# Performance work log

Measured on AMD Instinct MI355X. Metric: run time of the kernel, lower is better.

The kernel has to match this reference:

```python
import jax, jax.numpy as jnp
import numpy as np

HID = 1024
NH = 16
HD = 64
INTER = 2816
EPS = 1e-5


def _rms_norm(x, eps=EPS):
    x32 = x.astype(jnp.float32)
    var = jnp.mean(x32 * x32, axis=-1, keepdims=True)
    return (x32 * jax.lax.rsqrt(var + eps)).astype(x.dtype)


def _rotate_half(x):
    x1, x2 = jnp.split(x, 2, axis=-1)
    return jnp.concatenate([-x2, x1], axis=-1)


def setup_inputs() -> dict:
    key = jax.random.key(0)
    ks = jax.random.split(key, 6)
    B, S = 1, 2048
    # real RoPE tables: [S, HD]
    inv_freq = 1.0 / (10000.0 ** (np.arange(0, HD, 2, dtype=np.float32) / HD))
    t = np.arange(S, dtype=np.float32)
    freqs = np.outer(t, inv_freq)  # [S, HD/2]
    emb = np.concatenate([freqs, freqs], axis=-1)  # [S, HD]
    cos = jnp.asarray(np.cos(emb))
    sin = jnp.asarray(np.sin(emb))
    sc = 0.02
    return {
        "cos": cos,
        "sin": sin,
        "hidden_states": jax.random.normal(ks[0], (B, S, HID), jnp.float32),
        "attn_bias": jax.random.normal(ks[1], (B, NH, S, S), jnp.float32) * 0.1,
        "w_qkv": jax.random.normal(ks[2], (HID, (NH + 2 * NH) * HD), jnp.float32) * sc,
        "w_o": jax.random.normal(ks[3], (NH * HD, HID), jnp.float32) * sc,
        "w_gate_up": jax.random.normal(ks[4], (HID, 2 * INTER), jnp.float32) * sc,
        "w_down": jax.random.normal(ks[5], (INTER, HID), jnp.float32) * sc,
    }


def _attention(cos, sin, x, attn_bias, w_qkv, w_o):
    B, S, _ = x.shape
    qkv = (x @ w_qkv).reshape(B, S, 3 * NH, HD)
    q = qkv[:, :, :NH]          # [B,S,H,D]
    k = qkv[:, :, NH:2 * NH]
    v = qkv[:, :, 2 * NH:]
    c = cos[None, :, None, :]
    s = sin[None, :, None, :]
    q = q * c + _rotate_half(q) * s
    k = k * c + _rotate_half(k) * s
    scale = HD ** -0.5
    scores = jnp.einsum('bqhd,bkhd->bhqk', q, k) * scale + attn_bias
    attn = jax.nn.softmax(scores.astype(jnp.float32), axis=-1).astype(q.dtype)
    out = jnp.einsum('bhqk,bkhd->bqhd', attn, v).reshape(B, S, NH * HD)
    return out @ w_o


def _swiglu(x, w_gate_up, w_down):
    gu = x @ w_gate_up
    gate, up = jnp.split(gu, 2, axis=-1)
    return (jax.nn.silu(gate) * up) @ w_down


def reference(cos, sin, hidden_states, attn_bias, w_qkv, w_o, w_gate_up, w_down):
    x = hidden_states
    x = _rms_norm(x + _attention(cos, sin, x, attn_bias, w_qkv, w_o))
    x = _rms_norm(x + _swiglu(x, w_gate_up, w_down))
    return x
```

## Files before the change

### kernel.cpp

```cpp
#include <hip/hip_runtime.h>
#include <stdint.h>

using u16 = unsigned short;
typedef __bf16 bf16x8 __attribute__((ext_vector_type(8)));
typedef float f32x4 __attribute__((ext_vector_type(4)));

__device__ __forceinline__ u16 f2bf(float f) {
  union { float f; uint32_t u; } v; v.f = f;
  uint32_t r = v.u + 0x7fffu + ((v.u >> 16) & 1u);
  return (u16)(r >> 16);
}
__device__ __forceinline__ float bf2f(u16 h) {
  union { uint32_t u; float f; } v; v.u = ((uint32_t)h) << 16;
  return v.f;
}
__device__ __forceinline__ bf16x8 ldb8(const u16* p) {
  return *reinterpret_cast<const bf16x8*>(p);
}
__device__ __forceinline__ void gload_lds16(const void* g, void* l) {
  __builtin_amdgcn_global_load_lds(
      (const __attribute__((address_space(1))) void*)g,
      (__attribute__((address_space(3))) void*)l, 16, 0, 0);
}

__global__ __launch_bounds__(256) void prep_kernel(
    const float* __restrict__ w_qkv, const float* __restrict__ w_o,
    const float* __restrict__ w_gu, const float* __restrict__ w_down,
    const float* __restrict__ hidden, u16* __restrict__ wqkv_t,
    u16* __restrict__ wo_t, u16* __restrict__ wgu_t, u16* __restrict__ wd_t,
    u16* __restrict__ xb) {
  const int b = blockIdx.x;
  const int t = threadIdx.x;

  if (b >= 12544) {
    int idx = (b - 12544) * 256 + t;
    float4 v = *(const float4*)(hidden + (size_t)idx * 4);
    ushort4 o;
    o.x = f2bf(v.x); o.y = f2bf(v.y); o.z = f2bf(v.z); o.w = f2bf(v.w);
    *(ushort4*)(xb + (size_t)idx * 4) = o;
    return;
  }

  const float* W;
  u16* Wt;
  int N, K, lb;
  bool perm = false;
  if (b < 3072)      { W = w_qkv; Wt = wqkv_t; N = 3072; K = 1024; lb = b; }
  else if (b < 4096) { W = w_o;   Wt = wo_t;   N = 1024; K = 1024; lb = b - 3072; }
  else if (b < 9728) { W = w_gu;  Wt = wgu_t;  N = 5632; K = 1024; lb = b - 4096; perm = true; }
  else               { W = w_down; Wt = wd_t;  N = 1024; K = 2816; lb = b - 9728; }

  const int nx = N >> 5;
  const int n0 = (lb % nx) * 32, k0 = (lb / nx) * 32;
  const int tx = t & 31, ty = t >> 5;

  __shared__ u16 tile[32][33];
  const int nc = n0 + tx;
  const int src_col = perm ? (((nc & 1) == 0) ? (nc >> 1) : 2816 + (nc >> 1))
                           : nc;
#pragma unroll
  for (int i = 0; i < 32; i += 8)
    tile[ty + i][tx] = f2bf(W[(size_t)(k0 + ty + i) * N + src_col]);
  __syncthreads();
#pragma unroll
  for (int i = 0; i < 32; i += 8)
    Wt[(size_t)(n0 + ty + i) * K + k0 + tx] = tile[tx][ty + i];
}

__global__ __launch_bounds__(256) void gemm_qkv_rope(
    const u16* __restrict__ A, const u16* __restrict__ Bt,
    const float* __restrict__ cosb, const float* __restrict__ sinb,
    u16* __restrict__ qb, u16* __restrict__ kb, u16* __restrict__ vt,
    int M, int N, int K) {
  __shared__ __align__(16) u16 As[128 * 32];
  __shared__ __align__(16) u16 Bs[128 * 32];
  __shared__ u16 vbuf[4][64][17];
  const int tid = threadIdx.x;
  const int w = tid >> 6, lane = tid & 63;
  const int wr = w >> 1, wc = w & 1;
  const int r16 = lane & 15, g = lane >> 4;
  const int nwg = gridDim.x * gridDim.y;
  const int idx = blockIdx.y * gridDim.x + blockIdx.x;
  const int swz = (idx & 7) * (nwg >> 3) + (idx >> 3);
  const int m0 = (swz / gridDim.x) * 128, n0 = (swz % gridDim.x) * 128;
  const int ldrow = lane >> 2;
  const int ldk = (lane & 3) * 8;

  f32x4 acc[4][4] = {};

  for (int kt = 0; kt < K; kt += 32) {
#pragma unroll
    for (int i = 0; i < 2; ++i) {
      int chunk = w * 2 + i;
      int row = chunk * 16 + ldrow;
      gload_lds16(A + (size_t)(m0 + row) * K + kt + ldk, &As[chunk * 512]);
      gload_lds16(Bt + (size_t)(n0 + row) * K + kt + ldk, &Bs[chunk * 512]);
    }
    __syncthreads();
    bf16x8 a[4], b[4];
#pragma unroll
    for (int mt = 0; mt < 4; ++mt)
      a[mt] = ldb8(&As[(wr * 64 + mt * 16 + r16) * 32 + g * 8]);
#pragma unroll
    for (int nt = 0; nt < 4; ++nt)
      b[nt] = ldb8(&Bs[(wc * 64 + nt * 16 + r16) * 32 + g * 8]);
#pragma unroll
    for (int mt = 0; mt < 4; ++mt)
#pragma unroll
      for (int nt = 0; nt < 4; ++nt)
        acc[mt][nt] = __builtin_amdgcn_mfma_f32_16x16x32_bf16(
            a[mt], b[nt], acc[mt][nt], 0, 0, 0);
    __syncthreads();
  }

  const int type = n0 >> 10;
  const int head = ((n0 & 1023) >> 6) + wc;
  if (type < 2) {
    u16* outp = type == 0 ? qb : kb;
    const float qs = type == 0 ? 0.125f : 1.0f;
#pragma unroll
    for (int mt = 0; mt < 4; ++mt)
#pragma unroll
      for (int r = 0; r < 4; ++r) {
        const int srow = m0 + wr * 64 + mt * 16 + g * 4 + r;
#pragma unroll
        for (int nt = 0; nt < 4; ++nt) {
          const int d = nt * 16 + r16;
          float cv = cosb[srow * 64 + d];
          float sv = sinb[srow * 64 + d];
          float sgn = nt < 2 ? -1.f : 1.f;
          float val = acc[mt][nt][r] * cv + sgn * acc[mt][nt ^ 2][r] * sv;
          outp[((size_t)head * 2048 + srow) * 64 + d] = f2bf(val * qs);
        }
      }
  } else {
    const int s_base = m0 + wr * 64;
    const int d_lo = lane >> 4;
    (void)d_lo;
    const int dl = lane >> 2;
    const int sblk = (lane & 3) * 16;
#pragma unroll
    for (int nt = 0; nt < 4; ++nt) {
#pragma unroll
      for (int mt = 0; mt < 4; ++mt)
#pragma unroll
        for (int r = 0; r < 4; ++r)
          vbuf[w][mt * 16 + g * 4 + r][r16] = f2bf(acc[mt][nt][r]);
      u16* dst =
          vt + ((size_t)(head * 64 + nt * 16 + dl)) * 2048 + s_base + sblk;
#pragma unroll
      for (int jj = 0; jj < 4; ++jj) {
        ushort4 ov;
        ov.x = vbuf[w][sblk + jj * 4 + 0][dl];
        ov.y = vbuf[w][sblk + jj * 4 + 1][dl];
        ov.z = vbuf[w][sblk + jj * 4 + 2][dl];
        ov.w = vbuf[w][sblk + jj * 4 + 3][dl];
        *(ushort4*)(dst + jj * 4) = ov;
      }
    }
  }
}

__global__ __launch_bounds__(256) void gemm_bt_swiglu(
    const u16* __restrict__ A, const u16* __restrict__ Bt,
    u16* __restrict__ Hb, int M, int N, int K) {
  __shared__ __align__(16) u16 As[128 * 32];
  __shared__ __align__(16) u16 Bs[128 * 32];
  const int tid = threadIdx.x;
  const int w = tid >> 6, lane = tid & 63;
  const int wr = w >> 1, wc = w & 1;
  const int r16 = lane & 15, g = lane >> 4;
  const int nwg = gridDim.x * gridDim.y;
  const int idx = blockIdx.y * gridDim.x + blockIdx.x;
  const int swz = (idx & 7) * (nwg >> 3) + (idx >> 3);
  const int m0 = (swz / gridDim.x) * 128, n0 = (swz % gridDim.x) * 128;
  const int ldrow = lane >> 2;
  const int ldk = (lane & 3) * 8;

  f32x4 acc[4][4] = {};

  for (int kt = 0; kt < K; kt += 32) {
#pragma unroll
    for (int i = 0; i < 2; ++i) {
      int chunk = w * 2 + i;
      int row = chunk * 16 + ldrow;
      gload_lds16(A + (size_t)(m0 + row) * K + kt + ldk, &As[chunk * 512]);
      gload_lds16(Bt + (size_t)(n0 + row) * K + kt + ldk, &Bs[chunk * 512]);
    }
    __syncthreads();
    bf16x8 a[4], b[4];
#pragma unroll
    for (int mt = 0; mt < 4; ++mt)
      a[mt] = ldb8(&As[(wr * 64 + mt * 16 + r16) * 32 + g * 8]);
#pragma unroll
    for (int nt = 0; nt < 4; ++nt)
      b[nt] = ldb8(&Bs[(wc * 64 + nt * 16 + r16) * 32 + g * 8]);
#pragma unroll
    for (int mt = 0; mt < 4; ++mt)
#pragma unroll
      for (int nt = 0; nt < 4; ++nt)
        acc[mt][nt] = __builtin_amdgcn_mfma_f32_16x16x32_bf16(
            a[mt], b[nt], acc[mt][nt], 0, 0, 0);
    __syncthreads();
  }
#pragma unroll
  for (int mt = 0; mt < 4; ++mt)
#pragma unroll
    for (int nt = 0; nt < 4; ++nt)
#pragma unroll
      for (int r = 0; r < 4; ++r) {
        float val = acc[mt][nt][r];
        float other = __shfl_xor(val, 1);
        if ((r16 & 1) == 0) {
          float o = val / (1.f + __expf(-val)) * other;
          int row = m0 + wr * 64 + mt * 16 + g * 4 + r;
          int col = n0 + wc * 64 + nt * 16 + r16;
          Hb[(size_t)row * 2816 + (col >> 1)] = f2bf(o);
        }
      }
}

__global__ __launch_bounds__(256) void gemm_bt64(
    const u16* __restrict__ A, const u16* __restrict__ Bt,
    u16* __restrict__ C, int M, int N, int K) {
  __shared__ __align__(16) u16 As[64 * 32];
  __shared__ __align__(16) u16 Bs[128 * 32];
  const int tid = threadIdx.x;
  const int w = tid >> 6, lane = tid & 63;
  const int wr = w >> 1, wc = w & 1;
  const int r16 = lane & 15, g = lane >> 4;
  const int nwg = gridDim.x * gridDim.y;
  const int idx = blockIdx.y * gridDim.x + blockIdx.x;
  const int swz = (idx & 7) * (nwg >> 3) + (idx >> 3);
  const int m0 = (swz / gridDim.x) * 64, n0 = (swz % gridDim.x) * 128;
  const int ldrow = lane >> 2;
  const int ldk = (lane & 3) * 8;

  f32x4 acc[2][4] = {};

  for (int kt = 0; kt < K; kt += 32) {
#pragma unroll
    for (int i = 0; i < 3; ++i) {
      int chunk = w * 3 + i;
      if (chunk < 4) {
        int row = chunk * 16 + ldrow;
        gload_lds16(A + (size_t)(m0 + row) * K + kt + ldk, &As[chunk * 512]);
      } else {
        int cb = chunk - 4;
        int row = cb * 16 + ldrow;
        gload_lds16(Bt + (size_t)(n0 + row) * K + kt + ldk, &Bs[cb * 512]);
      }
    }
    __syncthreads();
    bf16x8 a[2], b[4];
#pragma unroll
    for (int mt = 0; mt < 2; ++mt)
      a[mt] = ldb8(&As[(wr * 32 + mt * 16 + r16) * 32 + g * 8]);
#pragma unroll
    for (int nt = 0; nt < 4; ++nt)
      b[nt] = ldb8(&Bs[(wc * 64 + nt * 16 + r16) * 32 + g * 8]);
#pragma unroll
    for (int mt = 0; mt < 2; ++mt)
#pragma unroll
      for (int nt = 0; nt < 4; ++nt)
        acc[mt][nt] = __builtin_amdgcn_mfma_f32_16x16x32_bf16(
            a[mt], b[nt], acc[mt][nt], 0, 0, 0);
    __syncthreads();
  }
#pragma unroll
  for (int mt = 0; mt < 2; ++mt)
#pragma unroll
    for (int nt = 0; nt < 4; ++nt)
#pragma unroll
      for (int r = 0; r < 4; ++r) {
        int row = m0 + wr * 32 + mt * 16 + g * 4 + r;
        int col = n0 + wc * 64 + nt * 16 + r16;
        C[(size_t)row * N + col] = f2bf(acc[mt][nt][r]);
      }
}

__global__ __launch_bounds__(256, 2) void attn_kernel(
    const u16* __restrict__ qb, const u16* __restrict__ kb,
    const u16* __restrict__ vt, const float* __restrict__ bias,
    u16* __restrict__ attnb) {
  const int bid = blockIdx.x;
  const int swz = (bid & 7) * 64 + (bid >> 3);
  const int h = swz >> 5;
  const int qt = swz & 31;
  const int tid = threadIdx.x;
  const int w = tid >> 6;
  const int lane = tid & 63;
  const int r16 = lane & 15, g = lane >> 4;

  __shared__ __align__(16) u16 P_lds[4][16 * 32];
  __shared__ float acc_s[4][16][64];
  __shared__ float m_s[4][16], l_s[4][16];

  bf16x8 qf0[4], qf1[4];
#pragma unroll
  for (int st = 0; st < 4; ++st) {
    const u16* qrow =
        qb + ((size_t)h * 2048 + qt * 64 + st * 16 + r16) * 64;
    qf0[st] = ldb8(qrow + g * 8);
    qf1[st] = ldb8(qrow + 32 + g * 8);
  }

  f32x4 acc[4][4] = {};
  float m[4][4], lsum[4][4];
#pragma unroll
  for (int st = 0; st < 4; ++st)
#pragma unroll
    for (int r = 0; r < 4; ++r) { m[st][r] = -1e30f; lsum[st][r] = 0.f; }

  const float* bbase = bias + ((size_t)h * 2048 + qt * 64) * 2048;

  const int kv0 = w * 512, kv1 = kv0 + 512;
  for (int kt = kv0; kt < kv1; kt += 32) {
    bf16x8 ka[2], kc[2];
#pragma unroll
    for (int c = 0; c < 2; ++c) {
      const u16* krow = kb + ((size_t)h * 2048 + kt + c * 16 + r16) * 64;
      ka[c] = ldb8(krow + g * 8);
      kc[c] = ldb8(krow + 32 + g * 8);
    }
    bf16x8 vf[4];
#pragma unroll
    for (int nt = 0; nt < 4; ++nt)
      vf[nt] =
          ldb8(vt + ((size_t)h * 64 + nt * 16 + r16) * 2048 + kt + g * 8);

#pragma unroll
    for (int st = 0; st < 4; ++st) {
      float bv[2][4];
#pragma unroll
      for (int c = 0; c < 2; ++c)
#pragma unroll
        for (int r = 0; r < 4; ++r)
          bv[c][r] = bbase[(size_t)(st * 16 + g * 4 + r) * 2048 + kt +
                           c * 16 + r16];

      f32x4 sc[2];
#pragma unroll
      for (int c = 0; c < 2; ++c) {
        f32x4 z = {0.f, 0.f, 0.f, 0.f};
        f32x4 t =
            __builtin_amdgcn_mfma_f32_16x16x32_bf16(qf0[st], ka[c], z, 0, 0, 0);
        sc[c] =
            __builtin_amdgcn_mfma_f32_16x16x32_bf16(qf1[st], kc[c], t, 0, 0, 0);
      }
#pragma unroll
      for (int c = 0; c < 2; ++c)
#pragma unroll
        for (int r = 0; r < 4; ++r)
          sc[c][r] += bv[c][r];

      float mnew[4];
#pragma unroll
      for (int r = 0; r < 4; ++r) {
        float t = fmaxf(sc[0][r], sc[1][r]);
        t = fmaxf(t, __shfl_xor(t, 1));
        t = fmaxf(t, __shfl_xor(t, 2));
        t = fmaxf(t, __shfl_xor(t, 4));
        t = fmaxf(t, __shfl_xor(t, 8));
        mnew[r] = fmaxf(m[st][r], t);
      }
#pragma unroll
      for (int r = 0; r < 4; ++r) {
        float p0 = __expf(sc[0][r] - mnew[r]);
        float p1 = __expf(sc[1][r] - mnew[r]);
        sc[0][r] = p0; sc[1][r] = p1;
        float alpha = __expf(m[st][r] - mnew[r]);
        lsum[st][r] = lsum[st][r] * alpha + (p0 + p1);
        m[st][r] = mnew[r];
#pragma unroll
        for (int nt = 0; nt < 4; ++nt) acc[st][nt][r] *= alpha;
      }
#pragma unroll
      for (int c = 0; c < 2; ++c)
#pragma unroll
        for (int r = 0; r < 4; ++r)
          P_lds[w][(g * 4 + r) * 32 + c * 16 + r16] = f2bf(sc[c][r]);
      bf16x8 pf = ldb8(&P_lds[w][r16 * 32 + g * 8]);
#pragma unroll
      for (int nt = 0; nt < 4; ++nt)
        acc[st][nt] = __builtin_amdgcn_mfma_f32_16x16x32_bf16(
            pf, vf[nt], acc[st][nt], 0, 0, 0);
    }
  }

#pragma unroll
  for (int st = 0; st < 4; ++st) {
    __syncthreads();
#pragma unroll
    for (int nt = 0; nt < 4; ++nt)
#pragma unroll
      for (int r = 0; r < 4; ++r)
        acc_s[w][g * 4 + r][nt * 16 + r16] = acc[st][nt][r];
    if (r16 == 0) {
#pragma unroll
      for (int r = 0; r < 4; ++r) m_s[w][g * 4 + r] = m[st][r];
    }
#pragma unroll
    for (int r = 0; r < 4; ++r) {
      float t = lsum[st][r];
      t += __shfl_xor(t, 1);
      t += __shfl_xor(t, 2);
      t += __shfl_xor(t, 4);
      t += __shfl_xor(t, 8);
      if (r16 == 0) l_s[w][g * 4 + r] = t;
    }
    __syncthreads();

    const int row = tid >> 4;
    const int col4 = (tid & 15) * 4;
    float m0v = m_s[0][row], m1v = m_s[1][row], m2v = m_s[2][row],
          m3v = m_s[3][row];
    float mm = fmaxf(fmaxf(m0v, m1v), fmaxf(m2v, m3v));
    float s0 = __expf(m0v - mm), s1 = __expf(m1v - mm);
    float s2 = __expf(m2v - mm), s3 = __expf(m3v - mm);
    float ltot = l_s[0][row] * s0 + l_s[1][row] * s1 + l_s[2][row] * s2 +
                 l_s[3][row] * s3;
    float inv = 1.f / ltot;
    ushort4 ov;
    u16* outp =
        attnb + (size_t)(qt * 64 + st * 16 + row) * 1024 + h * 64 + col4;
#pragma unroll
    for (int j = 0; j < 4; ++j) {
      float v = acc_s[0][row][col4 + j] * s0 + acc_s[1][row][col4 + j] * s1 +
                acc_s[2][row][col4 + j] * s2 + acc_s[3][row][col4 + j] * s3;
      ((u16*)&ov)[j] = f2bf(v * inv);
    }
    *(ushort4*)outp = ov;
  }
}

__global__ __launch_bounds__(256) void addnorm_kernel(
    const float* __restrict__ resid, const u16* __restrict__ delta,
    float* __restrict__ outf, u16* __restrict__ outb) {
  int row = blockIdx.x, tid = threadIdx.x;
  size_t base = (size_t)row * 1024 + tid * 4;
  float4 rv = *(const float4*)(resid + base);
  ushort4 dv = *(const ushort4*)(delta + base);
  float x0 = rv.x + bf2f(dv.x);
  float x1 = rv.y + bf2f(dv.y);
  float x2 = rv.z + bf2f(dv.z);
  float x3 = rv.w + bf2f(dv.w);
  float ss = x0 * x0 + x1 * x1 + x2 * x2 + x3 * x3;
#pragma unroll
  for (int sh = 32; sh >= 1; sh >>= 1) ss += __shfl_xor(ss, sh);
  __shared__ float red[4];
  if ((tid & 63) == 0) red[tid >> 6] = ss;
  __syncthreads();
  float tot = red[0] + red[1] + red[2] + red[3];
  float rstd = rsqrtf(tot * (1.0f / 1024.0f) + 1e-5f);
  float4 ov;
  ov.x = x0 * rstd; ov.y = x1 * rstd; ov.z = x2 * rstd; ov.w = x3 * rstd;
  *(float4*)(outf + base) = ov;
  if (outb) {
    ushort4 ob;
    ob.x = f2bf(ov.x); ob.y = f2bf(ov.y); ob.z = f2bf(ov.z); ob.w = f2bf(ov.w);
    *(ushort4*)(outb + base) = ob;
  }
}

extern "C" void kernel_launch(void* const* d_in, const int* in_sizes, int n_in,
                              void* d_out, int out_size, void* d_ws,
                              size_t ws_size, hipStream_t stream) {
  (void)in_sizes; (void)n_in; (void)out_size; (void)ws_size;
  const float* cosb  = (const float*)d_in[0];
  const float* sinb  = (const float*)d_in[1];
  const float* hidden = (const float*)d_in[2];
  const float* bias  = (const float*)d_in[3];
  const float* w_qkv = (const float*)d_in[4];
  const float* w_o   = (const float*)d_in[5];
  const float* w_gu  = (const float*)d_in[6];
  const float* w_down = (const float*)d_in[7];
  float* out = (float*)d_out;

  char* p = (char*)d_ws;
  auto alloc = [&](size_t bytes) {
    void* r = (void*)p;
    p += (bytes + 255) & ~(size_t)255;
    return r;
  };
  u16* wqkv_t = (u16*)alloc((size_t)3072 * 1024 * 2);
  u16* wo_t   = (u16*)alloc((size_t)1024 * 1024 * 2);
  u16* wgu_t  = (u16*)alloc((size_t)5632 * 1024 * 2);
  u16* wd_t   = (u16*)alloc((size_t)1024 * 2816 * 2);
  u16* xb     = (u16*)alloc((size_t)2048 * 1024 * 2);
  u16* qb     = (u16*)alloc((size_t)16 * 2048 * 64 * 2);
  u16* kb     = (u16*)alloc((size_t)16 * 2048 * 64 * 2);
  u16* vt     = (u16*)alloc((size_t)16 * 2048 * 64 * 2);
  u16* attnb  = (u16*)alloc((size_t)2048 * 1024 * 2);
  u16* ob     = (u16*)alloc((size_t)2048 * 1024 * 2);
  float* x1f  = (float*)alloc((size_t)2048 * 1024 * 4);
  u16* x1b    = (u16*)alloc((size_t)2048 * 1024 * 2);
  u16* hb     = (u16*)alloc((size_t)2048 * 2816 * 2);
  u16* mlpb   = (u16*)alloc((size_t)2048 * 1024 * 2);

  prep_kernel<<<14592, 256, 0, stream>>>(w_qkv, w_o, w_gu, w_down, hidden,
                                         wqkv_t, wo_t, wgu_t, wd_t, xb);

  gemm_qkv_rope<<<dim3(3072 / 128, 2048 / 128), 256, 0, stream>>>(
      xb, wqkv_t, cosb, sinb, qb, kb, vt, 2048, 3072, 1024);
  attn_kernel<<<512, 256, 0, stream>>>(qb, kb, vt, bias, attnb);
  gemm_bt64<<<dim3(1024 / 128, 2048 / 64), 256, 0, stream>>>(attnb, wo_t, ob, 2048, 1024, 1024);
  addnorm_kernel<<<2048, 256, 0, stream>>>(hidden, ob, x1f, x1b);
  gemm_bt_swiglu<<<dim3(5632 / 128, 2048 / 128), 256, 0, stream>>>(x1b, wgu_t, hb, 2048, 5632, 1024);
  gemm_bt64<<<dim3(1024 / 128, 2048 / 64), 256, 0, stream>>>(hb, wd_t, mlpb, 2048, 1024, 2816);
  addnorm_kernel<<<2048, 256, 0, stream>>>(x1f, mlpb, out, nullptr);
}
```

Measured before the change: 288.6 us.

## Shrink output GEMM tiles to 64x64 and widen attention KV step to 64

The o-proj and down-proj GEMMs move from 64x128 to 64x64 tiles, doubling the grid to 512 workgroups so more of the CUs are busy, at the cost of less operand reuse per tile. The attention inner loop now handles 64 keys per iteration instead of 32. K and V fragments are loaded inside the per-subtile loop, and the bias is read directly rather than prefetched, which halves the number of softmax max/rescale passes per key. This changes the register pressure and load scheduling in the attention kernel, and may add redundant K/V reloads across the four query subtiles.

Result: slower. 592.0 us (+105.1%).

```diff
diff --git a/kernel.cpp b/kernel.cpp
--- a/kernel.cpp
+++ b/kernel.cpp
@@ -135,8 +135,6 @@
       }
   } else {
     const int s_base = m0 + wr * 64;
-    const int d_lo = lane >> 4;
-    (void)d_lo;
     const int dl = lane >> 2;
     const int sblk = (lane & 3) * 16;
 #pragma unroll
@@ -220,11 +218,11 @@
       }
 }
 
-__global__ __launch_bounds__(256) void gemm_bt64(
+__global__ __launch_bounds__(256) void gemm_bt6464(
     const u16* __restrict__ A, const u16* __restrict__ Bt,
     u16* __restrict__ C, int M, int N, int K) {
   __shared__ __align__(16) u16 As[64 * 32];
-  __shared__ __align__(16) u16 Bs[128 * 32];
+  __shared__ __align__(16) u16 Bs[64 * 32];
   const int tid = threadIdx.x;
   const int w = tid >> 6, lane = tid & 63;
   const int wr = w >> 1, wc = w & 1;
@@ -232,16 +230,16 @@
   const int nwg = gridDim.x * gridDim.y;
   const int idx = blockIdx.y * gridDim.x + blockIdx.x;
   const int swz = (idx & 7) * (nwg >> 3) + (idx >> 3);
-  const int m0 = (swz / gridDim.x) * 64, n0 = (swz % gridDim.x) * 128;
+  const int m0 = (swz / gridDim.x) * 64, n0 = (swz % gridDim.x) * 64;
   const int ldrow = lane >> 2;
   const int ldk = (lane & 3) * 8;
 
-  f32x4 acc[2][4] = {};
+  f32x4 acc[2][2] = {};
 
   for (int kt = 0; kt < K; kt += 32) {
 #pragma unroll
-    for (int i = 0; i < 3; ++i) {
-      int chunk = w * 3 + i;
+    for (int i = 0; i < 2; ++i) {
+      int chunk = w * 2 + i;
       if (chunk < 4) {
         int row = chunk * 16 + ldrow;
         gload_lds16(A + (size_t)(m0 + row) * K + kt + ldk, &As[chunk * 512]);
@@ -252,17 +250,17 @@
       }
     }
     __syncthreads();
-    bf16x8 a[2], b[4];
+    bf16x8 a[2], b[2];
 #pragma unroll
     for (int mt = 0; mt < 2; ++mt)
       a[mt] = ldb8(&As[(wr * 32 + mt * 16 + r16) * 32 + g * 8]);
 #pragma unroll
-    for (int nt = 0; nt < 4; ++nt)
-      b[nt] = ldb8(&Bs[(wc * 64 + nt * 16 + r16) * 32 + g * 8]);
+    for (int nt = 0; nt < 2; ++nt)
+      b[nt] = ldb8(&Bs[(wc * 32 + nt * 16 + r16) * 32 + g * 8]);
 #pragma unroll
     for (int mt = 0; mt < 2; ++mt)
 #pragma unroll
-      for (int nt = 0; nt < 4; ++nt)
+      for (int nt = 0; nt < 2; ++nt)
         acc[mt][nt] = __builtin_amdgcn_mfma_f32_16x16x32_bf16(
             a[mt], b[nt], acc[mt][nt], 0, 0, 0);
     __syncthreads();
@@ -270,11 +268,11 @@
 #pragma unroll
   for (int mt = 0; mt < 2; ++mt)
 #pragma unroll
-    for (int nt = 0; nt < 4; ++nt)
+    for (int nt = 0; nt < 2; ++nt)
 #pragma unroll
       for (int r = 0; r < 4; ++r) {
         int row = m0 + wr * 32 + mt * 16 + g * 4 + r;
-        int col = n0 + wc * 64 + nt * 16 + r16;
+        int col = n0 + wc * 32 + nt * 16 + r16;
         C[(size_t)row * N + col] = f2bf(acc[mt][nt][r]);
       }
 }
@@ -315,49 +313,32 @@
   const float* bbase = bias + ((size_t)h * 2048 + qt * 64) * 2048;
 
   const int kv0 = w * 512, kv1 = kv0 + 512;
-  for (int kt = kv0; kt < kv1; kt += 32) {
-    bf16x8 ka[2], kc[2];
-#pragma unroll
-    for (int c = 0; c < 2; ++c) {
-      const u16* krow = kb + ((size_t)h * 2048 + kt + c * 16 + r16) * 64;
-      ka[c] = ldb8(krow + g * 8);
-      kc[c] = ldb8(krow + 32 + g * 8);
-    }
-    bf16x8 vf[4];
-#pragma unroll
-    for (int nt = 0; nt < 4; ++nt)
-      vf[nt] =
-          ldb8(vt + ((size_t)h * 64 + nt * 16 + r16) * 2048 + kt + g * 8);
-
+  for (int kt = kv0; kt < kv1; kt += 64) {
 #pragma unroll
     for (int st = 0; st < 4; ++st) {
-      float bv[2][4];
-#pragma unroll
-      for (int c = 0; c < 2; ++c)
-#pragma unroll
-        for (int r = 0; r < 4; ++r)
-          bv[c][r] = bbase[(size_t)(st * 16 + g * 4 + r) * 2048 + kt +
-                           c * 16 + r16];
-
-      f32x4 sc[2];
-#pragma unroll
-      for (int c = 0; c < 2; ++c) {
+      f32x4 sc[4];
+#pragma unroll
+      for (int c = 0; c < 4; ++c) {
+        const u16* krow = kb + ((size_t)h * 2048 + kt + c * 16 + r16) * 64;
+        bf16x8 k0 = ldb8(krow + g * 8);
+        bf16x8 k1 = ldb8(krow + 32 + g * 8);
         f32x4 z = {0.f, 0.f, 0.f, 0.f};
         f32x4 t =
-            __builtin_amdgcn_mfma_f32_16x16x32_bf16(qf0[st], ka[c], z, 0, 0, 0);
+            __builtin_amdgcn_mfma_f32_16x16x32_bf16(qf0[st], k0, z, 0, 0, 0);
         sc[c] =
-            __builtin_amdgcn_mfma_f32_16x16x32_bf16(qf1[st], kc[c], t, 0, 0, 0);
-      }
-#pragma unroll
-      for (int c = 0; c < 2; ++c)
+            __builtin_amdgcn_mfma_f32_16x16x32_bf16(qf1[st], k1, t, 0, 0, 0);
+      }
+#pragma unroll
+      for (int c = 0; c < 4; ++c)
 #pragma unroll
         for (int r = 0; r < 4; ++r)
-          sc[c][r] += bv[c][r];
+          sc[c][r] += bbase[(size_t)(st * 16 + g * 4 + r) * 2048 + kt +
+                            c * 16 + r16];
 
       float mnew[4];
 #pragma unroll
       for (int r = 0; r < 4; ++r) {
-        float t = fmaxf(sc[0][r], sc[1][r]);
+        float t = fmaxf(fmaxf(sc[0][r], sc[1][r]), fmaxf(sc[2][r], sc[3][r]));
         t = fmaxf(t, __shfl_xor(t, 1));
         t = fmaxf(t, __shfl_xor(t, 2));
         t = fmaxf(t, __shfl_xor(t, 4));
@@ -368,23 +349,33 @@
       for (int r = 0; r < 4; ++r) {
         float p0 = __expf(sc[0][r] - mnew[r]);
         float p1 = __expf(sc[1][r] - mnew[r]);
-        sc[0][r] = p0; sc[1][r] = p1;
+        float p2 = __expf(sc[2][r] - mnew[r]);
+        float p3 = __expf(sc[3][r] - mnew[r]);
+        sc[0][r] = p0; sc[1][r] = p1; sc[2][r] = p2; sc[3][r] = p3;
         float alpha = __expf(m[st][r] - mnew[r]);
-        lsum[st][r] = lsum[st][r] * alpha + (p0 + p1);
+        lsum[st][r] = lsum[st][r] * alpha + ((p0 + p1) + (p2 + p3));
         m[st][r] = mnew[r];
 #pragma unroll
         for (int nt = 0; nt < 4; ++nt) acc[st][nt][r] *= alpha;
       }
-#pragma unroll
-      for (int c = 0; c < 2; ++c)
-#pragma unroll
-        for (int r = 0; r < 4; ++r)
-          P_lds[w][(g * 4 + r) * 32 + c * 16 + r16] = f2bf(sc[c][r]);
-      bf16x8 pf = ldb8(&P_lds[w][r16 * 32 + g * 8]);
-#pragma unroll
-      for (int nt = 0; nt < 4; ++nt)
-        acc[st][nt] = __builtin_amdgcn_mfma_f32_16x16x32_bf16(
-            pf, vf[nt], acc[st][nt], 0, 0, 0);
+
+#pragma unroll
+      for (int half = 0; half < 2; ++half) {
+#pragma unroll
+        for (int c2 = 0; c2 < 2; ++c2)
+#pragma unroll
+          for (int r = 0; r < 4; ++r)
+            P_lds[w][(g * 4 + r) * 32 + c2 * 16 + r16] =
+                f2bf(sc[half * 2 + c2][r]);
+        bf16x8 pf = ldb8(&P_lds[w][r16 * 32 + g * 8]);
+#pragma unroll
+        for (int nt = 0; nt < 4; ++nt) {
+          bf16x8 vf = ldb8(vt + ((size_t)h * 64 + nt * 16 + r16) * 2048 +
+                           kt + half * 32 + g * 8);
+          acc[st][nt] = __builtin_amdgcn_mfma_f32_16x16x32_bf16(
+              pf, vf, acc[st][nt], 0, 0, 0);
+        }
+      }
     }
   }
 
@@ -504,9 +495,9 @@
   gemm_qkv_rope<<<dim3(3072 / 128, 2048 / 128), 256, 0, stream>>>(
       xb, wqkv_t, cosb, sinb, qb, kb, vt, 2048, 3072, 1024);
   attn_kernel<<<512, 256, 0, stream>>>(qb, kb, vt, bias, attnb);
-  gemm_bt64<<<dim3(1024 / 128, 2048 / 64), 256, 0, stream>>>(attnb, wo_t, ob, 2048, 1024, 1024);
+  gemm_bt6464<<<dim3(1024 / 64, 2048 / 64), 256, 0, stream>>>(attnb, wo_t, ob, 2048, 1024, 1024);
   addnorm_kernel<<<2048, 256, 0, stream>>>(hidden, ob, x1f, x1b);
   gemm_bt_swiglu<<<dim3(5632 / 128, 2048 / 128), 256, 0, stream>>>(x1b, wgu_t, hb, 2048, 5632, 1024);
-  gemm_bt64<<<dim3(1024 / 128, 2048 / 64), 256, 0, stream>>>(hb, wd_t, mlpb, 2048, 1024, 2816);
+  gemm_bt6464<<<dim3(1024 / 64, 2048 / 64), 256, 0, stream>>>(hb, wd_t, mlpb, 2048, 1024, 2816);
   addnorm_kernel<<<2048, 256, 0, stream>>>(x1f, mlpb, out, nullptr);
 }
```
